# Kernel optimization log

Measured on AMD Instinct MI355X. Metric: run time of the kernel, lower is better.

The kernel has to match this reference:

```python
import jax, jax.numpy as jnp
import numpy as np

B, N, E = 2, 2048, 1024
H = 16
D = E // H  # head dim = 64


def setup_inputs() -> dict:
    key = jax.random.key(0)
    ks = jax.random.split(key, 11)
    s = 1.0 / np.sqrt(E)
    return {
        "q": jax.random.normal(ks[0], (B, N, E), jnp.float32),
        "k": jax.random.normal(ks[1], (B, N, E), jnp.float32),
        "v": jax.random.normal(ks[2], (B, N, E), jnp.float32),
        "Wq": jax.random.normal(ks[3], (E, E), jnp.float32) * s,
        "bq": jnp.zeros((E,), jnp.float32),
        "Wk": jax.random.normal(ks[4], (E, E), jnp.float32) * s,
        "bk": jnp.zeros((E,), jnp.float32),
        "Wv": jax.random.normal(ks[5], (E, E), jnp.float32) * s,
        "bv": jnp.zeros((E,), jnp.float32),
        "Wo": jax.random.normal(ks[6], (E, E), jnp.float32) * s,
        "bo": jnp.zeros((E,), jnp.float32),
    }


def reference(q, k, v, Wq, bq, Wk, bk, Wv, bv, Wo, bo):
    # projections (torch Linear: x @ W^T + b)
    qp = q @ Wq.T + bq  # [B,N,E]
    kp = k @ Wk.T + bk
    vp = v @ Wv.T + bv
    # separate heads -> [B,H,N,D]
    qh = qp.reshape(B, N, H, D).transpose(0, 2, 1, 3)
    kh = kp.reshape(B, N, H, D).transpose(0, 2, 1, 3)
    vh = vp.reshape(B, N, H, D).transpose(0, 2, 1, 3)
    # scaled dot-product attention, full score matrix like the original
    scale = 1.0 / jnp.sqrt(jnp.asarray(D, qh.dtype))
    attn = jnp.einsum('bhqd,bhkd->bhqk', qh, kh) * scale
    attn = jax.nn.softmax(attn, axis=-1)
    out = jnp.einsum('bhqk,bhkd->bhqd', attn, vh)  # [B,H,N,D]
    # recombine heads
    out = out.transpose(0, 2, 1, 3).reshape(B, N, E)
    return out @ Wo.T + bo
```

## Files before the change

kernel.cpp:

```cpp
#include <hip/hip_runtime.h>

typedef _Float16 f16;
typedef __attribute__((ext_vector_type(2))) _Float16 f16x2;
typedef __attribute__((ext_vector_type(4))) _Float16 f16x4;
typedef __attribute__((ext_vector_type(8))) _Float16 f16x8;
typedef __attribute__((ext_vector_type(4))) float    f32x4;
typedef __attribute__((ext_vector_type(16))) float   f32x16;
typedef __attribute__((ext_vector_type(4))) unsigned u32x4;

static constexpr int B_ = 2, N_ = 2048, E_ = 1024, H_ = 16, D_ = 64;
static constexpr int M_ = B_ * N_;

#define MFMA16(a, b, c) __builtin_amdgcn_mfma_f32_16x16x32_f16(a, b, c, 0, 0, 0)
#define MFMA32(a, b, c) __builtin_amdgcn_mfma_f32_32x32x16_f16(a, b, c, 0, 0, 0)

#define QSCALE 0.18033688011112042f

__device__ __forceinline__ void gload_lds16(const f16* g, f16* l) {
    typedef __attribute__((address_space(1))) const unsigned gu32;
    typedef __attribute__((address_space(3))) unsigned       lu32;
    __builtin_amdgcn_global_load_lds((gu32*)g, (lu32*)l, 16, 0, 0);
}

__global__ __launch_bounds__(256) void castw_kernel(
    const float* __restrict__ Wq, const float* __restrict__ Wk,
    const float* __restrict__ Wv, const float* __restrict__ Wo,
    f16* __restrict__ dst)
{
    const int i = (blockIdx.x * 256 + threadIdx.x) * 4;
    const int which = i >> 20;
    const float* s = (which == 0) ? Wq : (which == 1) ? Wk : (which == 2) ? Wv : Wo;
    const int j = i & (E_ * E_ - 1);
    const f32x4 f = *(const f32x4*)&s[j];
    f16x4 o;
    o[0] = (f16)f[0]; o[1] = (f16)f[1]; o[2] = (f16)f[2]; o[3] = (f16)f[3];
    *(f16x4*)&dst[i] = o;
}

__global__ __launch_bounds__(256) void proj_gemm(
    const float* __restrict__ q, const float* __restrict__ k, const float* __restrict__ v,
    const f16* __restrict__ Wb,
    const float* __restrict__ bq, const float* __restrict__ bk, const float* __restrict__ bv,
    f16* __restrict__ qh, f16* __restrict__ kh, f16* __restrict__ vt)
{
    const int bid  = blockIdx.x;
    const int lin  = (bid & 7) * 96 + (bid >> 3);
    const int z    = lin >> 8;
    const int rem  = lin & 255;
    const int m0   = (rem >> 3) * 128;
    const int n0   = (rem & 7) * 128;

    const float* A    = (z == 0) ? q  : (z == 1) ? k  : v;
    const f16*   W    = Wb + (size_t)z * E_ * E_;
    const float* bias = (z == 0) ? bq : (z == 1) ? bk : bv;

    __shared__ f16 As[128][32];
    __shared__ f16 Bs[128][32];

    const int tid  = threadIdx.x;
    const int lane = tid & 63, w = tid >> 6;
    const int lr = lane & 15, lg = lane >> 4;
    const int wm = (w >> 1) * 64, wn = (w & 1) * 64;

    const int gch = ((lane & 3) ^ ((lane >> 3) & 3)) * 8;
    const f16* bg = W + (size_t)(n0 + w * 32 + (lane >> 2)) * E_ + gch;
    f16* bl0 = &Bs[w * 32][0];
    f16* bl1 = &Bs[w * 32 + 16][0];

    const int srow = tid >> 1;
    const int h    = tid & 1;
    const int s3   = srow & 3;
    const int c0   = (2 * h)     ^ s3;
    const int c1   = (2 * h + 1) ^ s3;
    const float* ag = A + (size_t)(m0 + srow) * E_;

    const int caA = (lg ^ (lr & 3)) * 8;
    const int caB = (lg ^ ((lr >> 1) & 3)) * 8;

    f32x4 acc[4][4];
#pragma unroll
    for (int i = 0; i < 4; i++)
#pragma unroll
        for (int j = 0; j < 4; j++) acc[i][j] = (f32x4){0.f, 0.f, 0.f, 0.f};

    f32x4 aA0 = *(const f32x4*)(ag + 8 * c0);
    f32x4 aA1 = *(const f32x4*)(ag + 8 * c0 + 4);
    f32x4 aB0 = *(const f32x4*)(ag + 8 * c1);
    f32x4 aB1 = *(const f32x4*)(ag + 8 * c1 + 4);

    for (int t = 0; t < E_ / 32; ++t) {
        __syncthreads();
        gload_lds16(bg,           bl0);
        gload_lds16(bg + 16 * E_, bl1);
        bg += 32;
        {
            f16x8 w0, w1;
#pragma unroll
            for (int j = 0; j < 4; j++) {
                w0[j] = (f16)aA0[j]; w0[4 + j] = (f16)aA1[j];
                w1[j] = (f16)aB0[j]; w1[4 + j] = (f16)aB1[j];
            }
            *(f16x8*)&As[srow][16 * h]     = w0;
            *(f16x8*)&As[srow][16 * h + 8] = w1;
        }
        if (t + 1 < E_ / 32) {
            const float* an = ag + (t + 1) * 32;
            aA0 = *(const f32x4*)(an + 8 * c0);
            aA1 = *(const f32x4*)(an + 8 * c0 + 4);
            aB0 = *(const f32x4*)(an + 8 * c1);
            aB1 = *(const f32x4*)(an + 8 * c1 + 4);
        }
        __syncthreads();

        f16x8 af[4], bfr[4];
#pragma unroll
        for (int ms = 0; ms < 4; ms++) af[ms]  = *(const f16x8*)&As[wm + ms * 16 + lr][caA];
#pragma unroll
        for (int ns = 0; ns < 4; ns++) bfr[ns] = *(const f16x8*)&Bs[wn + ns * 16 + lr][caB];
        __builtin_amdgcn_s_setprio(1);
#pragma unroll
        for (int ms = 0; ms < 4; ms++)
#pragma unroll
            for (int ns = 0; ns < 4; ns++)
                acc[ms][ns] = MFMA16(af[ms], bfr[ns], acc[ms][ns]);
        __builtin_amdgcn_s_setprio(0);
    }

    const float oscale = (z == 0) ? QSCALE : 1.0f;
#pragma unroll
    for (int ms = 0; ms < 4; ms++) {
        const int mbase = m0 + wm + ms * 16 + lg * 4;
#pragma unroll
        for (int ns = 0; ns < 4; ns++) {
            const int n  = n0 + wn + ns * 16 + lr;
            const float bn = bias[n];
            const int hh = n >> 6, dd = n & 63;
#pragma unroll
            for (int r = 0; r < 4; r++) {
                const float val = (acc[ms][ns][r] + bn) * oscale;
                const int mm = mbase + r;
                const int bb = mm >> 11;
                const int nn = mm & (N_ - 1);
                if (z == 2) {
                    vt[((size_t)(bb * H_ + hh) * D_ + dd) * N_ + nn] = (f16)val;
                } else {
                    f16* dst = (z == 0) ? qh : kh;
                    dst[((size_t)(bb * H_ + hh) * N_ + nn) * D_ + dd] = (f16)val;
                }
            }
        }
    }
}

__global__ __launch_bounds__(256) void attn_kernel(
    const f16* __restrict__ qh, const f16* __restrict__ kh,
    const f16* __restrict__ vt, f16* __restrict__ ao)
{
    const int bid = blockIdx.x;
    const int swz = (bid & 7) * 64 + (bid >> 3);
    const int qt = swz & 15;
    const int bh = swz >> 4;

    const int tid = threadIdx.x;
    const int w = tid >> 6, lane = tid & 63;
    const int l31 = lane & 31;
    const bool hi = (lane >> 5) != 0;
    const int hib = hi ? 1 : 0;

    const f16* qp = qh + (size_t)bh * N_ * D_;
    const f16* kp = kh + (size_t)bh * N_ * D_;
    const f16* vp = vt + (size_t)bh * D_ * N_;

    const int qrow = qt * 128 + w * 32 + l31;

    f16x8 qf[4];
#pragma unroll
    for (int ks = 0; ks < 4; ks++)
        qf[ks] = *(const f16x8*)&qp[(size_t)qrow * D_ + ks * 16 + hib * 8];

    __shared__ f16 Ks[2][64][64];
    __shared__ f16 Vs[2][64][64];

    const int srow = tid >> 3;
    const int sch  = tid & 7;
    const int ssl  = (sch ^ (srow & 7)) * 8;

    const f16* kg0 = kp + (size_t)srow * D_ + sch * 8;
    const f16* kg1 = kg0 + (size_t)32 * D_;
    const f16* vg0 = vp + (size_t)srow * N_ + sch * 8;
    const f16* vg1 = vg0 + (size_t)32 * N_;

    f32x16 oT0 = {0.f,0.f,0.f,0.f,0.f,0.f,0.f,0.f,0.f,0.f,0.f,0.f,0.f,0.f,0.f,0.f};
    f32x16 oT1 = oT0;
    float mrun = -3.0e38f, lrun = 0.f;

    f16x8 kr0 = *(const f16x8*)(kg0);
    f16x8 kr1 = *(const f16x8*)(kg1);
    f16x8 vr0 = *(const f16x8*)(vg0);
    f16x8 vr1 = *(const f16x8*)(vg1);

    constexpr int NT = N_ / 64;
    int cur = 0;

    for (int t = 0; t < NT; ++t) {
        *(f16x8*)&Ks[cur][srow     ][ssl] = kr0;
        *(f16x8*)&Ks[cur][srow + 32][ssl] = kr1;
        *(f16x8*)&Vs[cur][srow     ][ssl] = vr0;
        *(f16x8*)&Vs[cur][srow + 32][ssl] = vr1;
        if (t + 1 < NT) {
            kr0 = *(const f16x8*)(kg0 + (size_t)(t + 1) * 64 * D_);
            kr1 = *(const f16x8*)(kg1 + (size_t)(t + 1) * 64 * D_);
            vr0 = *(const f16x8*)(vg0 + (t + 1) * 64);
            vr1 = *(const f16x8*)(vg1 + (t + 1) * 64);
        }
        __syncthreads();

        f32x16 sA = {0.f,0.f,0.f,0.f,0.f,0.f,0.f,0.f,0.f,0.f,0.f,0.f,0.f,0.f,0.f,0.f};
        f32x16 sB = sA;
        __builtin_amdgcn_s_setprio(1);
#pragma unroll
        for (int ks = 0; ks < 4; ks++) {
            const int c = (ks * 2 + hib) ^ (l31 & 7);
            const f16x8 kfA = *(const f16x8*)&Ks[cur][l31     ][c * 8];
            const f16x8 kfB = *(const f16x8*)&Ks[cur][l31 + 32][c * 8];
            sA = MFMA32(kfA, qf[ks], sA);
            sB = MFMA32(kfB, qf[ks], sB);
        }
        __builtin_amdgcn_s_setprio(0);

        float t16[16];
#pragma unroll
        for (int r = 0; r < 16; r++) t16[r] = fmaxf(sA[r], sB[r]);
#pragma unroll
        for (int d = 8; d >= 1; d >>= 1)
#pragma unroll
            for (int r = 0; r < d; r++) t16[r] = fmaxf(t16[r], t16[r + d]);
        const float pmax = fmaxf(t16[0], __shfl_xor(t16[0], 32));

        if (!__all(pmax - mrun <= 8.0f)) {
            const float mnew = fmaxf(mrun, pmax);
            const float alpha = __builtin_amdgcn_exp2f(mrun - mnew);
            mrun = mnew;
            lrun *= alpha;
#pragma unroll
            for (int r = 0; r < 16; r++) { oT0[r] *= alpha; oT1[r] *= alpha; }
        }

        float p0 = 0.f, p1 = 0.f, p2 = 0.f, p3 = 0.f;
#pragma unroll
        for (int r = 0; r < 16; r += 4) {
            sA[r]   = __builtin_amdgcn_exp2f(sA[r]   - mrun); p0 += sA[r];
            sA[r+1] = __builtin_amdgcn_exp2f(sA[r+1] - mrun); p1 += sA[r+1];
            sA[r+2] = __builtin_amdgcn_exp2f(sA[r+2] - mrun); p2 += sA[r+2];
            sA[r+3] = __builtin_amdgcn_exp2f(sA[r+3] - mrun); p3 += sA[r+3];
        }
#pragma unroll
        for (int r = 0; r < 16; r += 4) {
            sB[r]   = __builtin_amdgcn_exp2f(sB[r]   - mrun); p0 += sB[r];
            sB[r+1] = __builtin_amdgcn_exp2f(sB[r+1] - mrun); p1 += sB[r+1];
            sB[r+2] = __builtin_amdgcn_exp2f(sB[r+2] - mrun); p2 += sB[r+2];
            sB[r+3] = __builtin_amdgcn_exp2f(sB[r+3] - mrun); p3 += sB[r+3];
        }
        float lsum = (p0 + p1) + (p2 + p3);
        lsum += __shfl_xor(lsum, 32);
        lrun += lsum;

        __builtin_amdgcn_s_setprio(1);
#define PVSTEP(PP0,PP1,PP2,PP3,PP4,PP5,PP6,PP7, KSI)                                   \
        {                                                                              \
            const unsigned w0 = __builtin_bit_cast(unsigned, __builtin_amdgcn_cvt_pkrtz(PP0, PP1)); \
            const unsigned w1 = __builtin_bit_cast(unsigned, __builtin_amdgcn_cvt_pkrtz(PP2, PP3)); \
            const unsigned w2 = __builtin_bit_cast(unsigned, __builtin_amdgcn_cvt_pkrtz(PP4, PP5)); \
            const unsigned w3 = __builtin_bit_cast(unsigned, __builtin_amdgcn_cvt_pkrtz(PP6, PP7)); \
            const unsigned x0 = (unsigned)__shfl_xor((int)w0, 32);                     \
            const unsigned x1 = (unsigned)__shfl_xor((int)w1, 32);                     \
            const unsigned x2 = (unsigned)__shfl_xor((int)w2, 32);                     \
            const unsigned x3 = (unsigned)__shfl_xor((int)w3, 32);                     \
            u32x4 pw;                                                                  \
            pw[0] = hi ? x2 : w0;                                                      \
            pw[1] = hi ? x3 : w1;                                                      \
            pw[2] = hi ? w2 : x0;                                                      \
            pw[3] = hi ? w3 : x1;                                                      \
            const f16x8 pa = __builtin_bit_cast(f16x8, pw);                            \
            const int c = ((KSI) * 2 + hib) ^ (l31 & 7);                               \
            const f16x8 vf0 = *(const f16x8*)&Vs[cur][l31     ][c * 8];                \
            const f16x8 vf1 = *(const f16x8*)&Vs[cur][l31 + 32][c * 8];                \
            oT0 = MFMA32(vf0, pa, oT0);                                                \
            oT1 = MFMA32(vf1, pa, oT1);                                                \
        }
        PVSTEP(sA[0],sA[1],sA[2],sA[3],sA[4],sA[5],sA[6],sA[7], 0)
        PVSTEP(sA[8],sA[9],sA[10],sA[11],sA[12],sA[13],sA[14],sA[15], 1)
        PVSTEP(sB[0],sB[1],sB[2],sB[3],sB[4],sB[5],sB[6],sB[7], 2)
        PVSTEP(sB[8],sB[9],sB[10],sB[11],sB[12],sB[13],sB[14],sB[15], 3)
#undef PVSTEP
        __builtin_amdgcn_s_setprio(0);

        cur ^= 1;
    }

    const float inv = 1.0f / lrun;
    const int b = bh >> 4, h = bh & 15;
    f16* dst = ao + (size_t)(b * N_ + qrow) * E_ + h * 64 + hib * 4;
#pragma unroll
    for (int g = 0; g < 4; g++) {
        f16x4 o0, o1;
#pragma unroll
        for (int j = 0; j < 4; j++) {
            o0[j] = (f16)(oT0[g * 4 + j] * inv);
            o1[j] = (f16)(oT1[g * 4 + j] * inv);
        }
        *(f16x4*)&dst[8 * g]      = o0;
        *(f16x4*)&dst[8 * g + 32] = o1;
    }
}

__global__ __launch_bounds__(256) void out_gemm(
    const f16* __restrict__ ao, const f16* __restrict__ Wo,
    const float* __restrict__ bo, float* __restrict__ out)
{
    __shared__ f16 As[128][32];
    __shared__ f16 Bs[128][32];

    const int bid = blockIdx.x;
    const int lin = (bid & 7) * 32 + (bid >> 3);
    const int m0  = (lin >> 3) * 128;
    const int n0  = (lin & 7) * 128;

    const int tid  = threadIdx.x;
    const int lane = tid & 63, w = tid >> 6;
    const int lr = lane & 15, lg = lane >> 4;
    const int wm = (w >> 1) * 64, wn = (w & 1) * 64;

    const int gch = ((lane & 3) ^ ((lane >> 3) & 3)) * 8;
    const f16* ag = ao + (size_t)(m0 + w * 32 + (lane >> 2)) * E_ + gch;
    const f16* bg = Wo + (size_t)(n0 + w * 32 + (lane >> 2)) * E_ + gch;
    f16* al0 = &As[w * 32][0];
    f16* al1 = &As[w * 32 + 16][0];
    f16* bl0 = &Bs[w * 32][0];
    f16* bl1 = &Bs[w * 32 + 16][0];

    const int ca = (lg ^ ((lr >> 1) & 3)) * 8;

    f32x4 acc[4][4];
#pragma unroll
    for (int i = 0; i < 4; i++)
#pragma unroll
        for (int j = 0; j < 4; j++) acc[i][j] = (f32x4){0.f, 0.f, 0.f, 0.f};

    for (int t = 0; t < E_ / 32; ++t) {
        __syncthreads();
        gload_lds16(ag,            al0);
        gload_lds16(ag + 16 * E_,  al1);
        gload_lds16(bg,            bl0);
        gload_lds16(bg + 16 * E_,  bl1);
        ag += 32; bg += 32;
        __syncthreads();

        f16x8 af[4], bfr[4];
#pragma unroll
        for (int ms = 0; ms < 4; ms++) af[ms]  = *(const f16x8*)&As[wm + ms * 16 + lr][ca];
#pragma unroll
        for (int ns = 0; ns < 4; ns++) bfr[ns] = *(const f16x8*)&Bs[wn + ns * 16 + lr][ca];
        __builtin_amdgcn_s_setprio(1);
#pragma unroll
        for (int ms = 0; ms < 4; ms++)
#pragma unroll
            for (int ns = 0; ns < 4; ns++)
                acc[ms][ns] = MFMA16(af[ms], bfr[ns], acc[ms][ns]);
        __builtin_amdgcn_s_setprio(0);
    }

#pragma unroll
    for (int ms = 0; ms < 4; ms++) {
        const int mbase = m0 + wm + ms * 16 + lg * 4;
#pragma unroll
        for (int ns = 0; ns < 4; ns++) {
            const int n = n0 + wn + ns * 16 + lr;
            const float bn = bo[n];
#pragma unroll
            for (int r = 0; r < 4; r++) {
                out[(size_t)(mbase + r) * E_ + n] = acc[ms][ns][r] + bn;
            }
        }
    }
}

extern "C" void kernel_launch(void* const* d_in, const int* in_sizes, int n_in,
                              void* d_out, int out_size, void* d_ws, size_t ws_size,
                              hipStream_t stream) {
    const float* q  = (const float*)d_in[0];
    const float* k  = (const float*)d_in[1];
    const float* v  = (const float*)d_in[2];
    const float* Wq = (const float*)d_in[3];
    const float* bq = (const float*)d_in[4];
    const float* Wk = (const float*)d_in[5];
    const float* bk = (const float*)d_in[6];
    const float* Wv = (const float*)d_in[7];
    const float* bv = (const float*)d_in[8];
    const float* Wo = (const float*)d_in[9];
    const float* bo = (const float*)d_in[10];
    float* out = (float*)d_out;

    char* ws = (char*)d_ws;
    f16* Wb = (f16*)ws;
    f16* qh = (f16*)(ws + (size_t)32 * 1024 * 1024);
    f16* kh = (f16*)(ws + (size_t)40 * 1024 * 1024);
    f16* vt = (f16*)(ws + (size_t)48 * 1024 * 1024);
    f16* ao = (f16*)(ws + (size_t)56 * 1024 * 1024);

    castw_kernel<<<4096, 256, 0, stream>>>(Wq, Wk, Wv, Wo, Wb);
    proj_gemm<<<768, 256, 0, stream>>>(q, k, v, Wb, bq, bk, bv, qh, kh, vt);
    attn_kernel<<<512, 256, 0, stream>>>(qh, kh, vt, ao);
    out_gemm<<<256, 256, 0, stream>>>(ao, Wb + (size_t)3 * E_ * E_, bo, out);
}
```

Measured before the change: 146.1 us.

## Double-buffer GEMM LDS tiles with register prefetch instead of direct-to-LDS loads

In both the projection and output GEMMs, the direct global-to-LDS loads are replaced by register prefetch of the next K-slice into double-buffered LDS tiles, which needs only one barrier per iteration. This removes the second __syncthreads and lets the next tile's global loads overlap the current MFMA work. In exchange it doubles LDS use, adds register pressure and VGPR-to-LDS store instructions, and gives up the asynchronous LDS-load path.

After: 146.5 us. Within noise of the previous version (+0.2%).

```diff
diff --git a/kernel.cpp b/kernel.cpp
--- a/kernel.cpp
+++ b/kernel.cpp
@@ -15,12 +15,6 @@
 #define MFMA32(a, b, c) __builtin_amdgcn_mfma_f32_32x32x16_f16(a, b, c, 0, 0, 0)
 
 #define QSCALE 0.18033688011112042f
-
-__device__ __forceinline__ void gload_lds16(const f16* g, f16* l) {
-    typedef __attribute__((address_space(1))) const unsigned gu32;
-    typedef __attribute__((address_space(3))) unsigned       lu32;
-    __builtin_amdgcn_global_load_lds((gu32*)g, (lu32*)l, 16, 0, 0);
-}
 
 __global__ __launch_bounds__(256) void castw_kernel(
     const float* __restrict__ Wq, const float* __restrict__ Wk,
@@ -54,25 +48,24 @@
     const f16*   W    = Wb + (size_t)z * E_ * E_;
     const float* bias = (z == 0) ? bq : (z == 1) ? bk : bv;
 
-    __shared__ f16 As[128][32];
-    __shared__ f16 Bs[128][32];
+    __shared__ f16 As[2][128][32];
+    __shared__ f16 Bs[2][128][32];
 
     const int tid  = threadIdx.x;
     const int lane = tid & 63, w = tid >> 6;
     const int lr = lane & 15, lg = lane >> 4;
     const int wm = (w >> 1) * 64, wn = (w & 1) * 64;
 
-    const int gch = ((lane & 3) ^ ((lane >> 3) & 3)) * 8;
-    const f16* bg = W + (size_t)(n0 + w * 32 + (lane >> 2)) * E_ + gch;
-    f16* bl0 = &Bs[w * 32][0];
-    f16* bl1 = &Bs[w * 32 + 16][0];
-
     const int srow = tid >> 1;
     const int h    = tid & 1;
-    const int s3   = srow & 3;
-    const int c0   = (2 * h)     ^ s3;
-    const int c1   = (2 * h + 1) ^ s3;
-    const float* ag = A + (size_t)(m0 + srow) * E_;
+    const int sA3  = srow & 3;
+    const int cA0  = (2 * h)     ^ sA3;
+    const int cA1  = (2 * h + 1) ^ sA3;
+    const int sB3  = (srow >> 1) & 3;
+    const int cB0  = (2 * h)     ^ sB3;
+    const int cB1  = (2 * h + 1) ^ sB3;
+    const float* ag  = A + (size_t)(m0 + srow) * E_;
+    const f16*   bgp = W + (size_t)(n0 + srow) * E_;
 
     const int caA = (lg ^ (lr & 3)) * 8;
     const int caB = (lg ^ ((lr >> 1) & 3)) * 8;
@@ -83,16 +76,17 @@
 #pragma unroll
         for (int j = 0; j < 4; j++) acc[i][j] = (f32x4){0.f, 0.f, 0.f, 0.f};
 
-    f32x4 aA0 = *(const f32x4*)(ag + 8 * c0);
-    f32x4 aA1 = *(const f32x4*)(ag + 8 * c0 + 4);
-    f32x4 aB0 = *(const f32x4*)(ag + 8 * c1);
-    f32x4 aB1 = *(const f32x4*)(ag + 8 * c1 + 4);
-
-    for (int t = 0; t < E_ / 32; ++t) {
-        __syncthreads();
-        gload_lds16(bg,           bl0);
-        gload_lds16(bg + 16 * E_, bl1);
-        bg += 32;
+    f32x4 aA0 = *(const f32x4*)(ag + 8 * cA0);
+    f32x4 aA1 = *(const f32x4*)(ag + 8 * cA0 + 4);
+    f32x4 aB0 = *(const f32x4*)(ag + 8 * cA1);
+    f32x4 aB1 = *(const f32x4*)(ag + 8 * cA1 + 4);
+    f16x8 bR0 = *(const f16x8*)(bgp + 8 * cB0);
+    f16x8 bR1 = *(const f16x8*)(bgp + 8 * cB1);
+
+    constexpr int NT = E_ / 32;
+    int cur = 0;
+
+    for (int t = 0; t < NT; ++t) {
         {
             f16x8 w0, w1;
 #pragma unroll
@@ -100,23 +94,28 @@
                 w0[j] = (f16)aA0[j]; w0[4 + j] = (f16)aA1[j];
                 w1[j] = (f16)aB0[j]; w1[4 + j] = (f16)aB1[j];
             }
-            *(f16x8*)&As[srow][16 * h]     = w0;
-            *(f16x8*)&As[srow][16 * h + 8] = w1;
-        }
-        if (t + 1 < E_ / 32) {
+            *(f16x8*)&As[cur][srow][16 * h]     = w0;
+            *(f16x8*)&As[cur][srow][16 * h + 8] = w1;
+            *(f16x8*)&Bs[cur][srow][16 * h]     = bR0;
+            *(f16x8*)&Bs[cur][srow][16 * h + 8] = bR1;
+        }
+        if (t + 1 < NT) {
             const float* an = ag + (t + 1) * 32;
-            aA0 = *(const f32x4*)(an + 8 * c0);
-            aA1 = *(const f32x4*)(an + 8 * c0 + 4);
-            aB0 = *(const f32x4*)(an + 8 * c1);
-            aB1 = *(const f32x4*)(an + 8 * c1 + 4);
+            const f16*   bn = bgp + (t + 1) * 32;
+            aA0 = *(const f32x4*)(an + 8 * cA0);
+            aA1 = *(const f32x4*)(an + 8 * cA0 + 4);
+            aB0 = *(const f32x4*)(an + 8 * cA1);
+            aB1 = *(const f32x4*)(an + 8 * cA1 + 4);
+            bR0 = *(const f16x8*)(bn + 8 * cB0);
+            bR1 = *(const f16x8*)(bn + 8 * cB1);
         }
         __syncthreads();
 
         f16x8 af[4], bfr[4];
 #pragma unroll
-        for (int ms = 0; ms < 4; ms++) af[ms]  = *(const f16x8*)&As[wm + ms * 16 + lr][caA];
-#pragma unroll
-        for (int ns = 0; ns < 4; ns++) bfr[ns] = *(const f16x8*)&Bs[wn + ns * 16 + lr][caB];
+        for (int ms = 0; ms < 4; ms++) af[ms]  = *(const f16x8*)&As[cur][wm + ms * 16 + lr][caA];
+#pragma unroll
+        for (int ns = 0; ns < 4; ns++) bfr[ns] = *(const f16x8*)&Bs[cur][wn + ns * 16 + lr][caB];
         __builtin_amdgcn_s_setprio(1);
 #pragma unroll
         for (int ms = 0; ms < 4; ms++)
@@ -124,6 +123,8 @@
             for (int ns = 0; ns < 4; ns++)
                 acc[ms][ns] = MFMA16(af[ms], bfr[ns], acc[ms][ns]);
         __builtin_amdgcn_s_setprio(0);
+
+        cur ^= 1;
     }
 
     const float oscale = (z == 0) ? QSCALE : 1.0f;
@@ -318,8 +319,8 @@
     const f16* __restrict__ ao, const f16* __restrict__ Wo,
     const float* __restrict__ bo, float* __restrict__ out)
 {
-    __shared__ f16 As[128][32];
-    __shared__ f16 Bs[128][32];
+    __shared__ f16 As[2][128][32];
+    __shared__ f16 Bs[2][128][32];
 
     const int bid = blockIdx.x;
     const int lin = (bid & 7) * 32 + (bid >> 3);
@@ -331,13 +332,13 @@
     const int lr = lane & 15, lg = lane >> 4;
     const int wm = (w >> 1) * 64, wn = (w & 1) * 64;
 
-    const int gch = ((lane & 3) ^ ((lane >> 3) & 3)) * 8;
-    const f16* ag = ao + (size_t)(m0 + w * 32 + (lane >> 2)) * E_ + gch;
-    const f16* bg = Wo + (size_t)(n0 + w * 32 + (lane >> 2)) * E_ + gch;
-    f16* al0 = &As[w * 32][0];
-    f16* al1 = &As[w * 32 + 16][0];
-    f16* bl0 = &Bs[w * 32][0];
-    f16* bl1 = &Bs[w * 32 + 16][0];
+    const int srow = tid >> 1;
+    const int h    = tid & 1;
+    const int s3   = (srow >> 1) & 3;
+    const int c0   = (2 * h)     ^ s3;
+    const int c1   = (2 * h + 1) ^ s3;
+    const f16* agp = ao + (size_t)(m0 + srow) * E_;
+    const f16* bgp = Wo + (size_t)(n0 + srow) * E_;
 
     const int ca = (lg ^ ((lr >> 1) & 3)) * 8;
 
@@ -347,20 +348,34 @@
 #pragma unroll
         for (int j = 0; j < 4; j++) acc[i][j] = (f32x4){0.f, 0.f, 0.f, 0.f};
 
-    for (int t = 0; t < E_ / 32; ++t) {
+    f16x8 aR0 = *(const f16x8*)(agp + 8 * c0);
+    f16x8 aR1 = *(const f16x8*)(agp + 8 * c1);
+    f16x8 bR0 = *(const f16x8*)(bgp + 8 * c0);
+    f16x8 bR1 = *(const f16x8*)(bgp + 8 * c1);
+
+    constexpr int NT = E_ / 32;
+    int cur = 0;
+
+    for (int t = 0; t < NT; ++t) {
+        *(f16x8*)&As[cur][srow][16 * h]     = aR0;
+        *(f16x8*)&As[cur][srow][16 * h + 8] = aR1;
+        *(f16x8*)&Bs[cur][srow][16 * h]     = bR0;
+        *(f16x8*)&Bs[cur][srow][16 * h + 8] = bR1;
+        if (t + 1 < NT) {
+            const f16* an = agp + (t + 1) * 32;
+            const f16* bn = bgp + (t + 1) * 32;
+            aR0 = *(const f16x8*)(an + 8 * c0);
+            aR1 = *(const f16x8*)(an + 8 * c1);
+            bR0 = *(const f16x8*)(bn + 8 * c0);
+            bR1 = *(const f16x8*)(bn + 8 * c1);
+        }
         __syncthreads();
-        gload_lds16(ag,            al0);
-        gload_lds16(ag + 16 * E_,  al1);
-        gload_lds16(bg,            bl0);
-        gload_lds16(bg + 16 * E_,  bl1);
-        ag += 32; bg += 32;
-        __syncthreads();
 
         f16x8 af[4], bfr[4];
 #pragma unroll
-        for (int ms = 0; ms < 4; ms++) af[ms]  = *(const f16x8*)&As[wm + ms * 16 + lr][ca];
-#pragma unroll
-        for (int ns = 0; ns < 4; ns++) bfr[ns] = *(const f16x8*)&Bs[wn + ns * 16 + lr][ca];
+        for (int ms = 0; ms < 4; ms++) af[ms]  = *(const f16x8*)&As[cur][wm + ms * 16 + lr][ca];
+#pragma unroll
+        for (int ns = 0; ns < 4; ns++) bfr[ns] = *(const f16x8*)&Bs[cur][wn + ns * 16 + lr][ca];
         __builtin_amdgcn_s_setprio(1);
 #pragma unroll
         for (int ms = 0; ms < 4; ms++)
@@ -368,6 +383,8 @@
             for (int ns = 0; ns < 4; ns++)
                 acc[ms][ns] = MFMA16(af[ms], bfr[ns], acc[ms][ns]);
         __builtin_amdgcn_s_setprio(0);
+
+        cur ^= 1;
     }
 
 #pragma unroll
```
